# Kernel tuning notes

Hardware: AMD Instinct MI355X
Metric: run time of the kernel (lower is better)

## Reference

```python
import jax, jax.numpy as jnp
import numpy as np

EPS = 1e-8

def _gn1(x, w, b):
    # GroupNorm(num_groups=1): normalize each sample over (C, T), per-channel affine.
    mean = jnp.mean(x, axis=(1, 2), keepdims=True)
    var = jnp.mean((x - mean) ** 2, axis=(1, 2), keepdims=True)
    xn = (x - mean) * jax.lax.rsqrt(var + EPS)
    return xn * w[None, :, None] + b[None, :, None]

def _film(h, e, gw, gb, bw, bb):
    # gamma/beta: Linear -> ReLU (dropout is identity in eval), broadcast over time.
    gamma = jax.nn.relu(e @ gw.T + gb)  # [B, C]
    beta = jax.nn.relu(e @ bw.T + bb)   # [B, C]
    return gamma[:, :, None] * h + beta[:, :, None]

def setup_inputs() -> dict:
    key = jax.random.key(0)
    ks = jax.random.split(key, 16)
    B, C, T = 16, 256, 16000
    s = lambda k, shape, scale: jax.random.normal(k, shape, dtype=jnp.float32) * scale
    return {
        "x": s(ks[0], (B, C, T), 1.0),
        "cue": s(ks[1], (B, 512), 1.0),
        "gn_a_w": jnp.ones((C,), jnp.float32), "gn_a_b": jnp.zeros((C,), jnp.float32),
        "gn_n_w": jnp.ones((C,), jnp.float32), "gn_n_b": jnp.zeros((C,), jnp.float32),
        "f1g_w": s(ks[2], (C, 512), 0.04), "f1g_b": jnp.zeros((C,), jnp.float32),
        "f1b_w": s(ks[3], (C, 512), 0.04), "f1b_b": jnp.zeros((C,), jnp.float32),
        "ln1_w": jnp.ones((C,), jnp.float32), "ln1_b": jnp.zeros((C,), jnp.float32),
        "conv1_w": s(ks[4], (128, C), 0.06),
        "cds_w": s(ks[5], (256, 512), 0.04),
        "f2g_w": s(ks[6], (128, 256), 0.06), "f2g_b": jnp.zeros((128,), jnp.float32),
        "f2b_w": s(ks[7], (128, 256), 0.06), "f2b_b": jnp.zeros((128,), jnp.float32),
        "ln2_w": jnp.ones((128,), jnp.float32), "ln2_b": jnp.zeros((128,), jnp.float32),
        "conv2_w": s(ks[8], (256, 128), 0.08),
    }

def reference(x, cue, gn_a_w, gn_a_b, gn_n_w, gn_n_b, f1g_w, f1g_b, f1b_w, f1b_b,
              ln1_w, ln1_b, conv1_w, cds_w, f2g_w, f2g_b, f2b_w, f2b_b,
              ln2_w, ln2_b, conv2_w):
    x = _gn1(x, gn_a_w, gn_a_b)                 # norm_audio (GroupNorm(1, C))
    x = _gn1(x, gn_n_w, gn_n_b)                 # norm (GroupNorm(1, C))
    x = _film(x, cue, f1g_w, f1g_b, f1b_w, f1b_b) + x  # film1 + residual
    x = _gn1(x, ln1_w, ln1_b)                   # layer_norm1
    x = jnp.einsum('bct,oc->bot', x, conv1_w)   # 1x1 Conv1d, no bias -> [B,128,T]
    cue2 = jax.nn.relu(cue @ cds_w.T)           # cue_down_sample2 -> [B,256]
    x = _film(x, cue2, f2g_w, f2g_b, f2b_w, f2b_b) + x  # film2 + residual
    x = _gn1(x, ln2_w, ln2_b)                   # layer_norm2
    x = jnp.einsum('bct,oc->bot', x, conv2_w)   # 1x1 Conv1d -> [B,256,T]
    return x
```

## Files before the change

### kernel.cpp

```cpp
#include <hip/hip_runtime.h>
#include <hip/hip_bf16.h>
#include <hip/hip_fp16.h>

#define T_LEN   16000
#define NB      16
#define NTT     250
#define NTB     125
#define EPSV    1e-8f

typedef _Float16 f16x8 __attribute__((ext_vector_type(8)));
typedef float    f32x4 __attribute__((ext_vector_type(4)));

__device__ __forceinline__ ushort f2h(float f) {
    _Float16 h = (_Float16)f;
    return *(ushort*)&h;
}
__device__ __forceinline__ float f4c(const float4& v, int i) {
    return i == 0 ? v.x : i == 1 ? v.y : i == 2 ? v.z : v.w;
}
__device__ __forceinline__ void gld16(const ushort* g, ushort* l) {
    __builtin_amdgcn_global_load_lds(
        (const __attribute__((address_space(1))) uint*)g,
        (__attribute__((address_space(3))) uint*)l, 16, 0, 0);
}
__device__ __forceinline__ float waveRed64(float v) {
    #pragma unroll
    for (int m = 1; m <= 32; m <<= 1) v += __shfl_xor(v, m, 64);
    return v;
}
__device__ __forceinline__ float4 ntload4(const float* p) {
    f32x4 v = __builtin_nontemporal_load((const f32x4*)p);
    return make_float4(v[0], v[1], v[2], v[3]);
}

__global__ __launch_bounds__(256) void kP1F(
    const float* __restrict__ x, ushort* __restrict__ Xp,
    float* __restrict__ sp, float* __restrict__ qp,
    const float* __restrict__ cue,
    const float* __restrict__ f1g_w, const float* __restrict__ f1g_b,
    const float* __restrict__ f1b_w, const float* __restrict__ f1b_b,
    const float* __restrict__ cds_w,
    float* __restrict__ G1, float* __restrict__ B1, float* __restrict__ CUE2)
{
    const int bid = blockIdx.x;
    if (bid < 256) {
        const int c = bid;
        const int lane = threadIdx.x & 63, w = threadIdx.x >> 6;
        const float4 wg0 = *(const float4*)(f1g_w + c*512 + lane*8);
        const float4 wg1 = *(const float4*)(f1g_w + c*512 + lane*8 + 4);
        const float4 wb0 = *(const float4*)(f1b_w + c*512 + lane*8);
        const float4 wb1 = *(const float4*)(f1b_w + c*512 + lane*8 + 4);
        const float4 wc0 = *(const float4*)(cds_w + c*512 + lane*8);
        const float4 wc1 = *(const float4*)(cds_w + c*512 + lane*8 + 4);
        #pragma unroll
        for (int bb = 0; bb < 4; ++bb) {
            const int b = w*4 + bb;
            const float4 u0 = *(const float4*)(cue + b*512 + lane*8);
            const float4 u1 = *(const float4*)(cue + b*512 + lane*8 + 4);
            float g = 0.f, bt = 0.f, cv = 0.f;
            #pragma unroll
            for (int i = 0; i < 4; ++i) {
                g  = fmaf(f4c(u0,i), f4c(wg0,i), g);  g  = fmaf(f4c(u1,i), f4c(wg1,i), g);
                bt = fmaf(f4c(u0,i), f4c(wb0,i), bt); bt = fmaf(f4c(u1,i), f4c(wb1,i), bt);
                cv = fmaf(f4c(u0,i), f4c(wc0,i), cv); cv = fmaf(f4c(u1,i), f4c(wc1,i), cv);
            }
            g = waveRed64(g); bt = waveRed64(bt); cv = waveRed64(cv);
            if (lane == 0) {
                G1[b*256 + c]   = fmaxf(g + f1g_b[c], 0.f) + 1.f;
                B1[b*256 + c]   = fmaxf(bt + f1b_b[c], 0.f);
                CUE2[b*256 + c] = fmaxf(cv, 0.f);
            }
        }
        return;
    }

    const int pb = bid - 256;
    const int b = pb / NTT, tt = pb % NTT;
    const int t0 = tt * 64;
    const int tid = threadIdx.x;
    const int cq = tid >> 2, jq = tid & 3;
    __shared__ __align__(16) ushort Hs[256][68];

    #pragma unroll
    for (int cc = 0; cc < 4; ++cc) {
        const int c = cc*64 + cq;
        float s4 = 0.f, q4 = 0.f;
        #pragma unroll
        for (int i = 0; i < 4; ++i) {
            const int ts = (jq + i*4)*4;
            const float4 v = ntload4(x + ((size_t)(b*256 + c))*T_LEN + t0 + ts);
            s4 += v.x + v.y + v.z + v.w;
            q4 += v.x*v.x + v.y*v.y + v.z*v.z + v.w*v.w;
            const ushort h0 = f2h(v.x), h1 = f2h(v.y), h2 = f2h(v.z), h3 = f2h(v.w);
            uint2 pk;
            pk.x = (uint)h0 | ((uint)h1 << 16);
            pk.y = (uint)h2 | ((uint)h3 << 16);
            *(uint2*)&Hs[c][ts] = pk;
        }
        s4 += __shfl_xor(s4, 1, 4); s4 += __shfl_xor(s4, 2, 4);
        q4 += __shfl_xor(q4, 1, 4); q4 += __shfl_xor(q4, 2, 4);
        if (jq == 0) {
            sp[((size_t)b*NTT + tt)*256 + c] = s4;
            qp[((size_t)b*NTT + tt)*256 + c] = q4;
        }
    }
    __syncthreads();
    ushort* dst = Xp + ((size_t)(b*NTT + tt)*4)*4096;
    #pragma unroll
    for (int k = 0; k < 8; ++k) {
        const int d  = tid + k*256;
        const int kc = d >> 9, r = d & 511;
        const int t  = r >> 3, us = r & 7;
        const int u  = us ^ (t & 7);
        const int c0 = kc*64 + u*8;
        uint4 val;
        val.x = (uint)Hs[c0+0][t] | ((uint)Hs[c0+1][t] << 16);
        val.y = (uint)Hs[c0+2][t] | ((uint)Hs[c0+3][t] << 16);
        val.z = (uint)Hs[c0+4][t] | ((uint)Hs[c0+5][t] << 16);
        val.w = (uint)Hs[c0+6][t] | ((uint)Hs[c0+7][t] << 16);
        *(uint4*)(dst + (size_t)d*8) = val;
    }
}

__device__ __forceinline__ float blockSum256(float v, float* red)
{
    #pragma unroll
    for (int off = 32; off; off >>= 1) v += __shfl_down(v, off, 64);
    __syncthreads();
    if ((threadIdx.x & 63) == 0) red[threadIdx.x >> 6] = v;
    __syncthreads();
    return red[0] + red[1] + red[2] + red[3];
}

__global__ __launch_bounds__(256) void kBM(
    const float* __restrict__ sp, const float* __restrict__ qp,
    const float* __restrict__ gn_a_w, const float* __restrict__ gn_a_b,
    const float* __restrict__ gn_n_w, const float* __restrict__ gn_n_b,
    const float* __restrict__ G1, const float* __restrict__ B1,
    const float* __restrict__ ln1_w, const float* __restrict__ ln1_b,
    const float* __restrict__ CUE2,
    const float* __restrict__ f2g_w, const float* __restrict__ f2g_b,
    const float* __restrict__ f2b_w, const float* __restrict__ f2b_b,
    const float* __restrict__ conv1_w,
    float* __restrict__ a4o, float* __restrict__ G2,
    float* __restrict__ E, ushort* __restrict__ Msf)
{
    const int b = blockIdx.x;
    const int c = threadIdx.x;
    __shared__ float red[4];
    __shared__ float sa4[256], sd4[256], sc2[256], sg2[16];

    float sc = 0.f, qc = 0.f;
    for (int i = 0; i < NTT; ++i) {
        sc += sp[((size_t)b*NTT + i)*256 + c];
        qc += qp[((size_t)b*NTT + i)*256 + c];
    }

    const float Ninv = 1.f / (256.f * 16000.f);
    const float Tf = 16000.f;

    float S  = blockSum256(sc, red);
    float Q  = blockSum256(qc, red);
    float mu1 = S * Ninv;
    float var1 = Q * Ninv - mu1 * mu1;
    float r1 = rsqrtf(var1 + EPSV);
    float a1 = gn_a_w[c] * r1;
    float d1 = gn_a_b[c] - mu1 * r1 * gn_a_w[c];

    float S2 = blockSum256(a1*sc + Tf*d1, red);
    float Q2 = blockSum256(a1*a1*qc + 2.f*a1*d1*sc + Tf*d1*d1, red);
    float mu2 = S2 * Ninv;
    float var2 = Q2 * Ninv - mu2 * mu2;
    float r2 = rsqrtf(var2 + EPSV);
    float wn = gn_n_w[c];
    float a2 = wn * r2 * a1;
    float d2 = wn * r2 * (d1 - mu2) + gn_n_b[c];

    const float g1 = G1[b*256 + c];
    const float b1 = B1[b*256 + c];
    float a3 = g1 * a2;
    float d3 = g1 * d2 + b1;

    float S3 = blockSum256(a3*sc + Tf*d3, red);
    float Q3 = blockSum256(a3*a3*qc + 2.f*a3*d3*sc + Tf*d3*d3, red);
    float mu3 = S3 * Ninv;
    float var3 = Q3 * Ninv - mu3 * mu3;
    float r3 = rsqrtf(var3 + EPSV);
    float w1 = ln1_w[c];
    const float a4v = w1 * r3 * a3;
    const float d4v = w1 * r3 * (d3 - mu3) + ln1_b[c];
    sa4[c] = a4v;
    sd4[c] = d4v;
    a4o[b*256 + c] = a4v;
    sc2[c] = CUE2[b*256 + c];
    __syncthreads();

    const int oi = c >> 4, l16 = c & 15;
    for (int og = 0; og < 8; ++og) {
        const int o = og*16 + oi;
        float g = 0.f, bt = 0.f, ed = 0.f;
        #pragma unroll
        for (int q = 0; q < 4; ++q) {
            const int k0 = l16*16 + q*4;
            const float4 a  = *(const float4*)(f2g_w  + o*256 + k0);
            const float4 bb = *(const float4*)(f2b_w  + o*256 + k0);
            const float4 cc = *(const float4*)(conv1_w + o*256 + k0);
            const float4 u  = *(const float4*)(&sc2[k0]);
            const float4 dd = *(const float4*)(&sd4[k0]);
            #pragma unroll
            for (int i = 0; i < 4; ++i) {
                g  = fmaf(f4c(u,i),  f4c(a,i),  g);
                bt = fmaf(f4c(u,i),  f4c(bb,i), bt);
                ed = fmaf(f4c(dd,i), f4c(cc,i), ed);
            }
        }
        #pragma unroll
        for (int m = 1; m <= 8; m <<= 1) {
            g  += __shfl_xor(g, m, 16);
            bt += __shfl_xor(bt, m, 16);
            ed += __shfl_xor(ed, m, 16);
        }
        if (l16 == 0) {
            const float G2v = fmaxf(g + f2g_b[o], 0.f) + 1.f;
            const float B2v = fmaxf(bt + f2b_b[o], 0.f);
            G2[b*128 + o] = G2v;
            E[b*128 + o]  = G2v * ed + B2v;
            sg2[oi] = G2v;
        }
        __syncthreads();
        const float av = sa4[c];
        #pragma unroll
        for (int i = 0; i < 16; ++i) {
            const int oo = og*16 + i;
            Msf[((size_t)b*128 + oo)*256 + c] = f2h(sg2[i] * conv1_w[oo*256 + c] * av);
        }
        __syncthreads();
    }
}

__global__ __launch_bounds__(256) void kC_gemm(
    const ushort* __restrict__ Xp, const ushort* __restrict__ Msf,
    const float* __restrict__ E,
    float* __restrict__ s2p, float* __restrict__ q2p)
{
    const int tb = blockIdx.x, b = blockIdx.y;
    const int tid = threadIdx.x, lane = tid & 63, w = tid >> 6;
    const int wo = w >> 1, wt = w & 1;
    const int sub = lane >> 4, li = lane & 15;
    const int o0 = wo * 64;
    __shared__ __align__(16) ushort Bs[2][8192];
    __shared__ float sSp[2][128], sQp[2][128];

    const ushort* src = Xp + ((size_t)(b*NTT + 2*tb)*4)*4096;
    const ushort* mp  = Msf + (size_t)b*128*256;

    f32x4 acc[4][4];
    #pragma unroll
    for (int i = 0; i < 4; ++i)
        #pragma unroll
        for (int jx = 0; jx < 4; ++jx) acc[i][jx] = (f32x4){0.f,0.f,0.f,0.f};

    #pragma unroll
    for (int jj = 0; jj < 4; ++jj) {
        const int m = w*4 + jj;
        const int ch = m >> 3, off = (m & 7)*512;
        gld16(src + (size_t)ch*16384 + off + lane*8, &Bs[0][ch*4096 + off]);
    }
    __syncthreads();
    for (int kc = 0; kc < 4; ++kc) {
        const int buf = kc & 1;
        if (kc < 3) {
            #pragma unroll
            for (int jj = 0; jj < 4; ++jj) {
                const int m = w*4 + jj;
                const int ch = m >> 3, off = (m & 7)*512;
                gld16(src + (size_t)ch*16384 + (kc+1)*4096 + off + lane*8,
                      &Bs[buf^1][ch*4096 + off]);
            }
        }
        f16x8 bfr[4][2];
        #pragma unroll
        for (int ft = 0; ft < 4; ++ft) {
            const int tl = ft*16 + li;
            #pragma unroll
            for (int ks = 0; ks < 2; ++ks) {
                const int u = (4*ks + sub) ^ (tl & 7);
                bfr[ft][ks] = *(const f16x8*)&Bs[buf][wt*4096 + tl*64 + u*8];
            }
        }
        #pragma unroll
        for (int ks = 0; ks < 2; ++ks) {
            #pragma unroll
            for (int fo = 0; fo < 4; ++fo) {
                const f16x8 a = *(const f16x8*)(mp + (size_t)(o0 + fo*16 + li)*256 + kc*64 + ks*32 + 8*sub);
                #pragma unroll
                for (int ft = 0; ft < 4; ++ft)
                    acc[fo][ft] = __builtin_amdgcn_mfma_f32_16x16x32_f16(a, bfr[ft][ks], acc[fo][ft], 0, 0, 0);
            }
        }
        __syncthreads();
    }

    #pragma unroll
    for (int fo = 0; fo < 4; ++fo) {
        #pragma unroll
        for (int r = 0; r < 4; ++r) {
            const int o = o0 + fo*16 + sub*4 + r;
            const float ev = E[b*128 + o];
            float sv = 0.f, qv = 0.f;
            #pragma unroll
            for (int ft = 0; ft < 4; ++ft) {
                const float z = acc[fo][ft][r] + ev;
                sv += z; qv += z*z;
            }
            #pragma unroll
            for (int m = 1; m <= 8; m <<= 1) {
                sv += __shfl_xor(sv, m, 64);
                qv += __shfl_xor(qv, m, 64);
            }
            if (li == 0) { sSp[wt][o] = sv; sQp[wt][o] = qv; }
        }
    }
    __syncthreads();
    if (tid < 128) {
        s2p[((size_t)b*NTB + tb)*128 + tid] = sSp[0][tid] + sSp[1][tid];
        q2p[((size_t)b*NTB + tb)*128 + tid] = sQp[0][tid] + sQp[1][tid];
    }
}

__global__ __launch_bounds__(256) void kD2_buildF(
    const float* __restrict__ s2p, const float* __restrict__ q2p,
    const float* __restrict__ ln2_w, const float* __restrict__ ln2_b,
    const float* __restrict__ Ev,
    const float* __restrict__ a4, const float* __restrict__ G2,
    const float* __restrict__ conv1_w, const float* __restrict__ conv2_w,
    ushort* __restrict__ Fsf, float* __restrict__ h)
{
    const int b = blockIdx.y, pg = blockIdx.x;
    const int tid = threadIdx.x;
    __shared__ float Qs[32][128];
    __shared__ float sA2[128], sAE[128];
    __shared__ float rS[2], rQ[2];

    float s = 0.f, qq = 0.f;
    if (tid < 128) {
        for (int tb = 0; tb < NTB; ++tb) {
            s  += s2p[((size_t)b*NTB + tb)*128 + tid];
            qq += q2p[((size_t)b*NTB + tb)*128 + tid];
        }
        float S = s, Q = qq;
        #pragma unroll
        for (int off = 32; off; off >>= 1) {
            S += __shfl_down(S, off, 64);
            Q += __shfl_down(Q, off, 64);
        }
        if ((tid & 63) == 0) { rS[tid >> 6] = S; rQ[tid >> 6] = Q; }
    }
    __syncthreads();
    const float N2inv = 1.f / (128.f * 16000.f);
    const float mu  = (rS[0] + rS[1]) * N2inv;
    const float var = (rQ[0] + rQ[1]) * N2inv - mu * mu;
    const float r = rsqrtf(var + EPSV);
    if (tid < 128) {
        const float a2v = ln2_w[tid] * r;
        const float d2v = ln2_b[tid] - mu * ln2_w[tid] * r;
        sA2[tid] = a2v;
        sAE[tid] = a2v * Ev[b*128 + tid] + d2v;
    }
    __syncthreads();

    #pragma unroll
    for (int k = 0; k < 16; ++k) {
        const int idx = tid + k*256;
        const int p = idx >> 7, o = idx & 127;
        Qs[p][o] = conv2_w[(pg*32 + p)*128 + o] * sA2[o] * G2[b*128 + o];
    }
    __syncthreads();
    float acc[32];
    #pragma unroll
    for (int p = 0; p < 32; ++p) acc[p] = 0.f;
    for (int o = 0; o < 128; ++o) {
        const float mv = conv1_w[o*256 + tid];
        #pragma unroll
        for (int p = 0; p < 32; ++p) acc[p] = fmaf(Qs[p][o], mv, acc[p]);
    }
    const float a = a4[b*256 + tid];
    #pragma unroll
    for (int p = 0; p < 32; ++p) {
        const size_t idx = ((size_t)b*256 + pg*32 + p)*256 + tid;
        Fsf[idx] = f2h(acc[p] * a);
    }
    if (tid < 32) {
        const int p = pg*32 + tid;
        float hv = 0.f;
        for (int o = 0; o < 128; ++o)
            hv += conv2_w[p*128 + o] * sAE[o];
        h[b*256 + p] = hv;
    }
}

__global__ __launch_bounds__(256) void kE_gemm(
    const ushort* __restrict__ Xp, const ushort* __restrict__ Fsf,
    const float* __restrict__ h, float* __restrict__ out)
{
    const int tt = blockIdx.x, b = blockIdx.y;
    const int tid = threadIdx.x, lane = tid & 63, w = tid >> 6;
    const int sub = lane >> 4, li = lane & 15;
    const int o0 = w * 64, t0 = tt * 64;
    __shared__ __align__(16) ushort Bs[2][4096];
    __shared__ __align__(16) float Ts[4][16][68];

    const ushort* src = Xp + ((size_t)(b*NTT + tt)*4)*4096;
    const ushort* fp  = Fsf + (size_t)b*65536;

    f32x4 acc[4][4];
    #pragma unroll
    for (int i = 0; i < 4; ++i)
        #pragma unroll
        for (int jx = 0; jx < 4; ++jx) acc[i][jx] = (f32x4){0.f,0.f,0.f,0.f};

    #pragma unroll
    for (int jj = 0; jj < 2; ++jj) {
        const int m = w*2 + jj;
        gld16(src + m*512 + lane*8, &Bs[0][m*512]);
    }
    __syncthreads();
    for (int kc = 0; kc < 4; ++kc) {
        const int buf = kc & 1;
        if (kc < 3) {
            #pragma unroll
            for (int jj = 0; jj < 2; ++jj) {
                const int m = w*2 + jj;
                gld16(src + (kc+1)*4096 + m*512 + lane*8, &Bs[buf^1][m*512]);
            }
        }
        f16x8 bfr[4][2];
        #pragma unroll
        for (int ft = 0; ft < 4; ++ft) {
            const int t = ft*16 + li;
            #pragma unroll
            for (int ks = 0; ks < 2; ++ks) {
                const int u = (4*ks + sub) ^ (t & 7);
                bfr[ft][ks] = *(const f16x8*)&Bs[buf][t*64 + u*8];
            }
        }
        #pragma unroll
        for (int ks = 0; ks < 2; ++ks) {
            #pragma unroll
            for (int fo = 0; fo < 4; ++fo) {
                const f16x8 a = *(const f16x8*)(fp + (size_t)(o0 + fo*16 + li)*256 + kc*64 + ks*32 + 8*sub);
                #pragma unroll
                for (int ft = 0; ft < 4; ++ft)
                    acc[fo][ft] = __builtin_amdgcn_mfma_f32_16x16x32_f16(a, bfr[ft][ks], acc[fo][ft], 0, 0, 0);
            }
        }
        __syncthreads();
    }

    #pragma unroll
    for (int fo = 0; fo < 4; ++fo) {
        float hv[4];
        #pragma unroll
        for (int r = 0; r < 4; ++r)
            hv[r] = h[b*256 + o0 + fo*16 + sub*4 + r];
        #pragma unroll
        for (int ft = 0; ft < 4; ++ft)
            #pragma unroll
            for (int r = 0; r < 4; ++r)
                Ts[w][sub*4 + r][ft*16 + li] = acc[fo][ft][r] + hv[r];
        #pragma unroll
        for (int it = 0; it < 4; ++it) {
            const int row = it*4 + sub;
            const f32x4 v = *(const f32x4*)&Ts[w][row][li*4];
            __builtin_nontemporal_store(v,
                (f32x4*)(out + ((size_t)(b*256 + o0 + fo*16 + row))*T_LEN + t0 + li*4));
        }
    }
}

extern "C" void kernel_launch(void* const* d_in, const int* in_sizes, int n_in,
                              void* d_out, int out_size, void* d_ws, size_t ws_size,
                              hipStream_t stream)
{
    const float* x       = (const float*)d_in[0];
    const float* cue     = (const float*)d_in[1];
    const float* gn_a_w  = (const float*)d_in[2];
    const float* gn_a_b  = (const float*)d_in[3];
    const float* gn_n_w  = (const float*)d_in[4];
    const float* gn_n_b  = (const float*)d_in[5];
    const float* f1g_w   = (const float*)d_in[6];
    const float* f1g_b   = (const float*)d_in[7];
    const float* f1b_w   = (const float*)d_in[8];
    const float* f1b_b   = (const float*)d_in[9];
    const float* ln1_w   = (const float*)d_in[10];
    const float* ln1_b   = (const float*)d_in[11];
    const float* conv1_w = (const float*)d_in[12];
    const float* cds_w   = (const float*)d_in[13];
    const float* f2g_w   = (const float*)d_in[14];
    const float* f2g_b   = (const float*)d_in[15];
    const float* f2b_w   = (const float*)d_in[16];
    const float* f2b_b   = (const float*)d_in[17];
    const float* ln2_w   = (const float*)d_in[18];
    const float* ln2_b   = (const float*)d_in[19];
    const float* conv2_w = (const float*)d_in[20];
    float* out = (float*)d_out;

    float* ws = (float*)d_ws;
    float*  sp   = ws;
    float*  qp   = ws + 1024000;
    float*  G1   = ws + 2048000;
    float*  B1   = ws + 2052096;
    float*  CUE2 = ws + 2056192;
    float*  G2   = ws + 2060288;
    float*  a4   = ws + 2062336;
    float*  E    = ws + 2066432;
    float*  h    = ws + 2068480;
    float*  s2p  = ws + 2072576;
    float*  q2p  = ws + 2328576;
    ushort* Msf  = (ushort*)(ws + 2584576);
    ushort* Fsf  = (ushort*)(ws + 2846720);
    ushort* Xp   = (ushort*)(ws + 3371008);

    kP1F<<<256 + NTT*NB, 256, 0, stream>>>(x, Xp, sp, qp,
        cue, f1g_w, f1g_b, f1b_w, f1b_b, cds_w, G1, B1, CUE2);

    kBM<<<NB, 256, 0, stream>>>(sp, qp, gn_a_w, gn_a_b, gn_n_w, gn_n_b,
                                G1, B1, ln1_w, ln1_b, CUE2,
                                f2g_w, f2g_b, f2b_w, f2b_b, conv1_w,
                                a4, G2, E, Msf);

    kC_gemm<<<dim3(NTB, NB), 256, 0, stream>>>(Xp, Msf, E, s2p, q2p);

    kD2_buildF<<<dim3(8, NB), 256, 0, stream>>>(s2p, q2p, ln2_w, ln2_b, E,
                                                a4, G2, conv1_w, conv2_w,
                                                Fsf, h);

    kE_gemm<<<dim3(NTT, NB), 256, 0, stream>>>(Xp, Fsf, h, out);
}
```

Before: 315.2 us.

## Parallelize stats reduction and load full K tile upfront in both GEMMs

```diff
diff --git a/kernel.cpp b/kernel.cpp
--- a/kernel.cpp
+++ b/kernel.cpp
@@ -122,6 +122,30 @@
     }
 }
 
+__global__ __launch_bounds__(256) void kR_reduce(
+    const float* __restrict__ sp, const float* __restrict__ qp,
+    float* __restrict__ s1, float* __restrict__ q1)
+{
+    const int cg = blockIdx.x, b = blockIdx.y;
+    const int ci = threadIdx.x & 31, ig = threadIdx.x >> 5;
+    const int c = cg*32 + ci;
+    float s = 0.f, q = 0.f;
+    for (int i = ig; i < NTT; i += 8) {
+        s += sp[((size_t)b*NTT + i)*256 + c];
+        q += qp[((size_t)b*NTT + i)*256 + c];
+    }
+    __shared__ float rs[8][32], rq[8][32];
+    rs[ig][ci] = s; rq[ig][ci] = q;
+    __syncthreads();
+    if (threadIdx.x < 32) {
+        float ss = 0.f, qq = 0.f;
+        #pragma unroll
+        for (int g = 0; g < 8; ++g) { ss += rs[g][threadIdx.x]; qq += rq[g][threadIdx.x]; }
+        s1[b*256 + cg*32 + threadIdx.x] = ss;
+        q1[b*256 + cg*32 + threadIdx.x] = qq;
+    }
+}
+
 __device__ __forceinline__ float blockSum256(float v, float* red)
 {
     #pragma unroll
@@ -133,7 +157,7 @@
 }
 
 __global__ __launch_bounds__(256) void kBM(
-    const float* __restrict__ sp, const float* __restrict__ qp,
+    const float* __restrict__ s1, const float* __restrict__ q1,
     const float* __restrict__ gn_a_w, const float* __restrict__ gn_a_b,
     const float* __restrict__ gn_n_w, const float* __restrict__ gn_n_b,
     const float* __restrict__ G1, const float* __restrict__ B1,
@@ -150,11 +174,8 @@
     __shared__ float red[4];
     __shared__ float sa4[256], sd4[256], sc2[256], sg2[16];
 
-    float sc = 0.f, qc = 0.f;
-    for (int i = 0; i < NTT; ++i) {
-        sc += sp[((size_t)b*NTT + i)*256 + c];
-        qc += qp[((size_t)b*NTT + i)*256 + c];
-    }
+    const float sc = s1[b*256 + c];
+    const float qc = q1[b*256 + c];
 
     const float Ninv = 1.f / (256.f * 16000.f);
     const float Tf = 16000.f;
@@ -248,7 +269,7 @@
     const int wo = w >> 1, wt = w & 1;
     const int sub = lane >> 4, li = lane & 15;
     const int o0 = wo * 64;
-    __shared__ __align__(16) ushort Bs[2][8192];
+    __shared__ __align__(16) ushort Bs[32768];
     __shared__ float sSp[2][128], sQp[2][128];
 
     const ushort* src = Xp + ((size_t)(b*NTT + 2*tb)*4)*4096;
@@ -261,65 +282,47 @@
         for (int jx = 0; jx < 4; ++jx) acc[i][jx] = (f32x4){0.f,0.f,0.f,0.f};
 
     #pragma unroll
-    for (int jj = 0; jj < 4; ++jj) {
-        const int m = w*4 + jj;
-        const int ch = m >> 3, off = (m & 7)*512;
-        gld16(src + (size_t)ch*16384 + off + lane*8, &Bs[0][ch*4096 + off]);
-    }
-    __syncthreads();
-    for (int kc = 0; kc < 4; ++kc) {
-        const int buf = kc & 1;
-        if (kc < 3) {
-            #pragma unroll
-            for (int jj = 0; jj < 4; ++jj) {
-                const int m = w*4 + jj;
-                const int ch = m >> 3, off = (m & 7)*512;
-                gld16(src + (size_t)ch*16384 + (kc+1)*4096 + off + lane*8,
-                      &Bs[buf^1][ch*4096 + off]);
-            }
-        }
-        f16x8 bfr[4][2];
+    for (int m = 0; m < 16; ++m) {
+        const int off = m*2048 + w*512;
+        gld16(src + off + lane*8, &Bs[off]);
+    }
+    __syncthreads();
+
+    #pragma unroll
+    for (int ks = 0; ks < 8; ++ks) {
+        const int kc = ks >> 1;
+        const int uo = (ks & 1)*4 + sub;
+        f16x8 xf[4];
         #pragma unroll
         for (int ft = 0; ft < 4; ++ft) {
             const int tl = ft*16 + li;
+            xf[ft] = *(const f16x8*)&Bs[(wt*4 + kc)*4096 + tl*64 + (uo ^ (tl & 7))*8];
+        }
+        const int k8 = kc*64 + (ks & 1)*32 + 8*sub;
+        #pragma unroll
+        for (int fo = 0; fo < 4; ++fo) {
+            const f16x8 mf = *(const f16x8*)(mp + (size_t)(o0 + fo*16 + li)*256 + k8);
             #pragma unroll
-            for (int ks = 0; ks < 2; ++ks) {
-                const int u = (4*ks + sub) ^ (tl & 7);
-                bfr[ft][ks] = *(const f16x8*)&Bs[buf][wt*4096 + tl*64 + u*8];
-            }
-        }
-        #pragma unroll
-        for (int ks = 0; ks < 2; ++ks) {
+            for (int ft = 0; ft < 4; ++ft)
+                acc[ft][fo] = __builtin_amdgcn_mfma_f32_16x16x32_f16(xf[ft], mf, acc[ft][fo], 0, 0, 0);
+        }
+    }
+
+    #pragma unroll
+    for (int fo = 0; fo < 4; ++fo) {
+        const int o = o0 + fo*16 + li;
+        const float ev = E[b*128 + o];
+        float sv = 0.f, qv = 0.f;
+        #pragma unroll
+        for (int ft = 0; ft < 4; ++ft)
             #pragma unroll
-            for (int fo = 0; fo < 4; ++fo) {
-                const f16x8 a = *(const f16x8*)(mp + (size_t)(o0 + fo*16 + li)*256 + kc*64 + ks*32 + 8*sub);
-                #pragma unroll
-                for (int ft = 0; ft < 4; ++ft)
-                    acc[fo][ft] = __builtin_amdgcn_mfma_f32_16x16x32_f16(a, bfr[ft][ks], acc[fo][ft], 0, 0, 0);
-            }
-        }
-        __syncthreads();
-    }
-
-    #pragma unroll
-    for (int fo = 0; fo < 4; ++fo) {
-        #pragma unroll
-        for (int r = 0; r < 4; ++r) {
-            const int o = o0 + fo*16 + sub*4 + r;
-            const float ev = E[b*128 + o];
-            float sv = 0.f, qv = 0.f;
-            #pragma unroll
-            for (int ft = 0; ft < 4; ++ft) {
-                const float z = acc[fo][ft][r] + ev;
+            for (int r = 0; r < 4; ++r) {
+                const float z = acc[ft][fo][r] + ev;
                 sv += z; qv += z*z;
             }
-            #pragma unroll
-            for (int m = 1; m <= 8; m <<= 1) {
-                sv += __shfl_xor(sv, m, 64);
-                qv += __shfl_xor(qv, m, 64);
-            }
-            if (li == 0) { sSp[wt][o] = sv; sQp[wt][o] = qv; }
-        }
+        sv += __shfl_xor(sv, 16, 64); sv += __shfl_xor(sv, 32, 64);
+        qv += __shfl_xor(qv, 16, 64); qv += __shfl_xor(qv, 32, 64);
+        if (sub == 0) { sSp[wt][o] = sv; sQp[wt][o] = qv; }
     }
     __syncthreads();
     if (tid < 128) {
@@ -407,8 +410,7 @@
     const int tid = threadIdx.x, lane = tid & 63, w = tid >> 6;
     const int sub = lane >> 4, li = lane & 15;
     const int o0 = w * 64, t0 = tt * 64;
-    __shared__ __align__(16) ushort Bs[2][4096];
-    __shared__ __align__(16) float Ts[4][16][68];
+    __shared__ __align__(16) ushort Bs[16384];
 
     const ushort* src = Xp + ((size_t)(b*NTT + tt)*4)*4096;
     const ushort* fp  = Fsf + (size_t)b*65536;
@@ -420,60 +422,45 @@
         for (int jx = 0; jx < 4; ++jx) acc[i][jx] = (f32x4){0.f,0.f,0.f,0.f};
 
     #pragma unroll
-    for (int jj = 0; jj < 2; ++jj) {
-        const int m = w*2 + jj;
-        gld16(src + m*512 + lane*8, &Bs[0][m*512]);
-    }
-    __syncthreads();
-    for (int kc = 0; kc < 4; ++kc) {
-        const int buf = kc & 1;
-        if (kc < 3) {
+    for (int m = 0; m < 8; ++m) {
+        const int off = m*2048 + w*512;
+        gld16(src + off + lane*8, &Bs[off]);
+    }
+    __syncthreads();
+
+    #pragma unroll
+    for (int ks = 0; ks < 8; ++ks) {
+        const int kc = ks >> 1;
+        const int uo = (ks & 1)*4 + sub;
+        f16x8 xf[4];
+        #pragma unroll
+        for (int ft = 0; ft < 4; ++ft) {
+            const int tl = ft*16 + li;
+            xf[ft] = *(const f16x8*)&Bs[kc*4096 + tl*64 + (uo ^ (tl & 7))*8];
+        }
+        const int k8 = kc*64 + (ks & 1)*32 + 8*sub;
+        #pragma unroll
+        for (int fo = 0; fo < 4; ++fo) {
+            const f16x8 ff = *(const f16x8*)(fp + (size_t)(o0 + fo*16 + li)*256 + k8);
             #pragma unroll
-            for (int jj = 0; jj < 2; ++jj) {
-                const int m = w*2 + jj;
-                gld16(src + (kc+1)*4096 + m*512 + lane*8, &Bs[buf^1][m*512]);
-            }
-        }
-        f16x8 bfr[4][2];
+            for (int ft = 0; ft < 4; ++ft)
+                acc[ft][fo] = __builtin_amdgcn_mfma_f32_16x16x32_f16(xf[ft], ff, acc[ft][fo], 0, 0, 0);
+        }
+    }
+
+    #pragma unroll
+    for (int fo = 0; fo < 4; ++fo) {
+        const int o = o0 + fo*16 + li;
+        const float hv = h[b*256 + o];
+        float* obase = out + ((size_t)(b*256 + o))*T_LEN + t0;
         #pragma unroll
         for (int ft = 0; ft < 4; ++ft) {
-            const int t = ft*16 + li;
-            #pragma unroll
-            for (int ks = 0; ks < 2; ++ks) {
-                const int u = (4*ks + sub) ^ (t & 7);
-                bfr[ft][ks] = *(const f16x8*)&Bs[buf][t*64 + u*8];
-            }
-        }
-        #pragma unroll
-        for (int ks = 0; ks < 2; ++ks) {
-            #pragma unroll
-            for (int fo = 0; fo < 4; ++fo) {
-                const f16x8 a = *(const f16x8*)(fp + (size_t)(o0 + fo*16 + li)*256 + kc*64 + ks*32 + 8*sub);
-                #pragma unroll
-                for (int ft = 0; ft < 4; ++ft)
-                    acc[fo][ft] = __builtin_amdgcn_mfma_f32_16x16x32_f16(a, bfr[ft][ks], acc[fo][ft], 0, 0, 0);
-            }
-        }
-        __syncthreads();
-    }
-
-    #pragma unroll
-    for (int fo = 0; fo < 4; ++fo) {
-        float hv[4];
-        #pragma unroll
-        for (int r = 0; r < 4; ++r)
-            hv[r] = h[b*256 + o0 + fo*16 + sub*4 + r];
-        #pragma unroll
-        for (int ft = 0; ft < 4; ++ft)
-            #pragma unroll
-            for (int r = 0; r < 4; ++r)
-                Ts[w][sub*4 + r][ft*16 + li] = acc[fo][ft][r] + hv[r];
-        #pragma unroll
-        for (int it = 0; it < 4; ++it) {
-            const int row = it*4 + sub;
-            const f32x4 v = *(const f32x4*)&Ts[w][row][li*4];
-            __builtin_nontemporal_store(v,
-                (f32x4*)(out + ((size_t)(b*256 + o0 + fo*16 + row))*T_LEN + t0 + li*4));
+            f32x4 v;
+            v[0] = acc[ft][fo][0] + hv;
+            v[1] = acc[ft][fo][1] + hv;
+            v[2] = acc[ft][fo][2] + hv;
+            v[3] = acc[ft][fo][3] + hv;
+            __builtin_nontemporal_store(v, (f32x4*)(obase + ft*16 + sub*4));
         }
     }
 }
@@ -515,16 +502,20 @@
     float*  a4   = ws + 2062336;
     float*  E    = ws + 2066432;
     float*  h    = ws + 2068480;
-    float*  s2p  = ws + 2072576;
-    float*  q2p  = ws + 2328576;
-    ushort* Msf  = (ushort*)(ws + 2584576);
-    ushort* Fsf  = (ushort*)(ws + 2846720);
-    ushort* Xp   = (ushort*)(ws + 3371008);
+    float*  s1   = ws + 2072576;
+    float*  q1   = ws + 2076672;
+    float*  s2p  = ws + 2080768;
+    float*  q2p  = ws + 2336768;
+    ushort* Msf  = (ushort*)(ws + 2592768);
+    ushort* Fsf  = (ushort*)(ws + 2854912);
+    ushort* Xp   = (ushort*)(ws + 3379200);
 
     kP1F<<<256 + NTT*NB, 256, 0, stream>>>(x, Xp, sp, qp,
         cue, f1g_w, f1g_b, f1b_w, f1b_b, cds_w, G1, B1, CUE2);
 
-    kBM<<<NB, 256, 0, stream>>>(sp, qp, gn_a_w, gn_a_b, gn_n_w, gn_n_b,
+    kR_reduce<<<dim3(8, NB), 256, 0, stream>>>(sp, qp, s1, q1);
+
+    kBM<<<NB, 256, 0, stream>>>(s1, q1, gn_a_w, gn_a_b, gn_n_w, gn_n_b,
                                 G1, B1, ln1_w, ln1_b, CUE2,
                                 f2g_w, f2g_b, f2b_w, f2b_b, conv1_w,
                                 a4, G2, E, Msf);
```

Measured after the change: 317.2 us. About the same (+0.7%).
